# Kernel tuning notes

Measured on AMD Instinct MI355X. Metric: run time of the kernel, lower is better.

## Reference

```python
import jax, jax.numpy as jnp
import numpy as np
from jax import lax

H = 256  # hidden_dim
NDIM = 3
K = 32   # k_neighbors


def sincos_embed(coords, dim, ndim):
    # ContinuousSinCosEmbed: per-coordinate sin/cos features, zero-padded to `dim`.
    dpn = dim // ndim          # channels per coordinate
    half = dpn // 2
    freqs = 1.0 / (10000.0 ** (jnp.arange(half, dtype=coords.dtype) / half))
    ang = coords[..., :, None] * freqs                      # (..., ndim, half)
    emb = jnp.concatenate([jnp.sin(ang), jnp.cos(ang)], -1)  # (..., ndim, 2*half)
    emb = emb.reshape(coords.shape[:-1] + (ndim * 2 * half,))
    pad = dim - ndim * 2 * half
    if pad:
        emb = jnp.concatenate([emb, jnp.zeros(emb.shape[:-1] + (pad,), emb.dtype)], -1)
    return emb


def setup_inputs() -> dict:
    key = jax.random.key(0)
    ks = jax.random.split(key, 8)
    N, S = 50000, 1024
    positions = jax.random.uniform(ks[0], (N, NDIM), dtype=jnp.float32) * 10.0
    supernode_indices = jax.random.randint(ks[1], (S,), 0, N, dtype=jnp.int32)
    g = 1.0 / np.sqrt(H)
    W1 = jax.random.normal(ks[2], (H, H), jnp.float32) * g
    b1 = jnp.zeros((H,), jnp.float32)
    W2 = jax.random.normal(ks[3], (H, H), jnp.float32) * g
    b2 = jnp.zeros((H,), jnp.float32)
    Wp = jax.random.normal(ks[4], (2 * H, H), jnp.float32) * (1.0 / np.sqrt(2 * H))
    bp = jnp.zeros((H,), jnp.float32)
    return {"positions": positions, "supernode_indices": supernode_indices,
            "W1": W1, "b1": b1, "W2": W2, "b2": b2, "Wp": Wp, "bp": bp}


def reference(positions, supernode_indices, W1, b1, W2, b2, Wp, bp):
    # positions: (N, 3); supernode_indices: (S,)
    sup_pos = positions[supernode_indices]                 # (S, 3)
    # kNN neighbor search via dense pairwise squared distances (memory-bound)
    diff = sup_pos[:, None, :] - positions[None, :, :]     # (S, N, 3)
    dist2 = jnp.sum(diff * diff, axis=-1)                  # (S, N)
    _, nbr_idx = lax.top_k(-dist2, K)                      # (S, K)
    nbr_pos = positions[nbr_idx]                           # (S, K, 3)
    # relpos mode: embed (relative position, distance) -> ndim+1 = 4 coords
    rel = sup_pos[:, None, :] - nbr_pos                    # (S, K, 3)
    d = jnp.sqrt(jnp.sum(rel * rel, axis=-1, keepdims=True))  # (S, K, 1)
    rel_feat = jnp.concatenate([rel, d], axis=-1)          # (S, K, 4)
    msg_in = sincos_embed(rel_feat, H, NDIM + 1)           # (S, K, H)
    # message MLP: Dense -> gelu -> Dense
    h = jax.nn.gelu(jnp.einsum('ski,ij->skj', msg_in, W1) + b1)
    msgs = jnp.einsum('ski,ij->skj', h, W2) + b2           # (S, K, H)
    # scatter-reduce: mean over neighbors per supernode
    agg = jnp.mean(msgs, axis=1)                           # (S, H)
    # supernode absolute position embedding, concat, project
    sup_emb = sincos_embed(sup_pos, H, NDIM)               # (S, H)
    feats = jnp.concatenate([sup_emb, agg], axis=-1)       # (S, 2H)
    out = feats @ Wp + bp                                  # (S, H)
    return out[None]                                        # (1, S, H)
```

## Files before the change

kernel.cpp:

```cpp
#include <hip/hip_runtime.h>
#include <hip/hip_bf16.h>
#include <math.h>

typedef short bf16x8 __attribute__((ext_vector_type(8)));
typedef float f32x4  __attribute__((ext_vector_type(4)));

constexpr int   H     = 256;
constexpr int   KNB   = 32;
constexpr int   TPB   = 512;
constexpr int   GC    = 16;
constexpr float HINV  = 1.6f;
constexpr float HCEL  = 0.625f;
constexpr int   SLOTS = 32;
constexpr int   OCAP  = 256;
constexpr int   CAP   = 512;

__device__ __forceinline__ ushort f2bf(float x) {
    unsigned u = __float_as_uint(x);
    u += 0x7FFF + ((u >> 16) & 1);
    return (ushort)(u >> 16);
}

__device__ __forceinline__ float gelu_fast(float x) {
    float u = 0.7978845608028654f * (x + 0.044715f * x * x * x);
    float t = exp2f(-2.885390081777927f * u);
    return x / (1.0f + t);
}

__device__ __forceinline__ int cell_of(float x, float y, float z) {
    int cx = min(GC - 1, max(0, (int)(x * HINV)));
    int cy = min(GC - 1, max(0, (int)(y * HINV)));
    int cz = min(GC - 1, max(0, (int)(z * HINV)));
    return (cz * GC + cy) * GC + cx;
}

__global__ __launch_bounds__(256)
void prep(const float* __restrict__ W1, const float* __restrict__ pos, int N,
          ushort* __restrict__ W1t, float4* __restrict__ pos4s,
          int* __restrict__ origidx, int* __restrict__ cellcnt,
          int* __restrict__ ovfidx, float4* __restrict__ ovfpos) {
    const int b = blockIdx.x;
    if (b < 64) {
        __shared__ float tile[32][33];
        const int ti = b >> 3, tj = b & 7;
        const int r  = threadIdx.x >> 5, c = threadIdx.x & 31;
#pragma unroll
        for (int rr = r; rr < 32; rr += 8)
            tile[rr][c] = W1[(ti * 32 + rr) * H + tj * 32 + c];
        __syncthreads();
#pragma unroll
        for (int rr = r; rr < 32; rr += 8) {
            int j = tj * 32 + rr;
            W1t[j * H + ti * 32 + c] = f2bf(tile[c][rr]);
        }
    } else {
        int i = (b - 64) * 256 + threadIdx.x;
        if (i < N) {
            float x = pos[3 * i], y = pos[3 * i + 1], z = pos[3 * i + 2];
            float4 P = make_float4(x, y, z, 0.f);
            int c = cell_of(x, y, z);
            int slot = atomicAdd(&cellcnt[c], 1);
            if (slot < SLOTS) {
                pos4s[c * SLOTS + slot] = P;
                origidx[c * SLOTS + slot] = i;
            } else {
                int o = atomicAdd(&cellcnt[4096], 1);
                if (o < OCAP) { ovfpos[o] = P; ovfidx[o] = i; }
            }
        }
    }
}

__global__ __launch_bounds__(TPB, 8)
void fused_knn_mlp(const float* __restrict__ pos,
                   const float4* __restrict__ pos4s,
                   const int* __restrict__ origidx,
                   const int* __restrict__ cellcnt,
                   const int* __restrict__ ovfidx, const float4* __restrict__ ovfpos,
                   const int* __restrict__ supidx,
                   const ushort* __restrict__ W1t, const float* __restrict__ b1,
                   const float* __restrict__ W2, const float* __restrict__ b2,
                   float* __restrict__ featsM)
{
    __shared__ __align__(16) char pool[16384];
    float* amaxd = (float*)pool;
    int*   acnt  = (int*)(pool + 512);
    int*   ccell = (int*)(pool + 1024);
    int*   ccnt  = (int*)(pool + 2048);
    float* cmnd  = (float*)(pool + 3072);
    int*   cpre  = (int*)(pool + 4096);
    float* d2buf = (float*)(pool + 5120);
    int*   obuf  = (int*)(pool + 7168);
    float* pxb   = (float*)(pool + 9216);
    float* pyb   = (float*)(pool + 11264);
    float* pzb   = (float*)(pool + 13312);
    ushort* msg  = (ushort*)pool;
    float*  p2   = (float*)pool;

    __shared__ float rf[KNB][5];
    __shared__ int   selo[KNB];
    __shared__ float hb[H];
    __shared__ int   wsum[4];
    __shared__ float tau2_sh, tau32_sh;
    __shared__ int   cnt_sh, ncl;

    const int s    = blockIdx.x;
    const int t    = threadIdx.x;
    const int lane = t & 63;
    const int w    = t >> 6;

    const int sidx = supidx[s];
    const float sx = pos[3 * sidx], sy = pos[3 * sidx + 1], sz = pos[3 * sidx + 2];

    constexpr float L2_10000 = 13.287712379549449f;

    if (t == 0) { ncl = 0; tau2_sh = 301.f; }

    const int scx = min(GC - 1, max(0, (int)(sx * HINV)));
    const int scy = min(GC - 1, max(0, (int)(sy * HINV)));
    const int scz = min(GC - 1, max(0, (int)(sz * HINV)));
    const int ax0 = max(0, scx - 2), ax1 = min(GC - 1, scx + 2);
    const int ay0 = max(0, scy - 2), ay1 = min(GC - 1, scy + 2);
    const int az0 = max(0, scz - 2), az1 = min(GC - 1, scz + 2);
    const int anx = ax1 - ax0 + 1, any_ = ay1 - ay0 + 1, anz = az1 - az0 + 1;
    const int an  = anx * any_ * anz;
    if (t < an) {
        int ci = t;
        int X = ax0 + ci % anx, rem = ci / anx;
        int Y = ay0 + rem % any_, Z = az0 + rem / any_;
        int cell = (Z * GC + Y) * GC + X;
        acnt[ci] = min(cellcnt[cell], SLOTS);
        float lx = X * HCEL, ly = Y * HCEL, lz = Z * HCEL;
        float mx = fmaxf(fabsf(sx - lx), fabsf(lx + HCEL - sx));
        float my = fmaxf(fabsf(sy - ly), fabsf(ly + HCEL - sy));
        float mz = fmaxf(fabsf(sz - lz), fabsf(lz + HCEL - sz));
        amaxd[ci] = mx * mx + my * my + mz * mz;
    }

    if (t < 256) {
        float se = 0.f;
        if (t < 252) {
            int c  = t / 84;
            int rr = t - c * 84;
            int f  = (rr < 42) ? rr : rr - 42;
            float coord = (c == 0) ? sx : ((c == 1) ? sy : sz);
            float ang = coord * exp2f(-(float)f * (L2_10000 / 42.f));
            se = (rr < 42) ? __sinf(ang) : __cosf(ang);
        }
        featsM[s * (2 * H) + t] = se;
    }
    __syncthreads();
    if (t < an) {
        int ci = t;
        float myv = amaxd[ci];
        int Sc = 0;
        for (int j = 0; j < an; j++) {
            bool less = (amaxd[j] < myv) || (amaxd[j] == myv && j < ci);
            Sc += less ? acnt[j] : 0;
        }
        if (Sc < KNB && KNB <= Sc + acnt[ci]) tau2_sh = myv;
    }
    __syncthreads();
    const float tau2 = tau2_sh;
    const float R2 = tau2 + 1e-3f;
    const float R  = sqrtf(R2);
    if (t == 0) tau32_sh = R2;

    const int bx0 = max(0, (int)floorf((sx - R) * HINV));
    const int bx1 = min(GC - 1, (int)floorf((sx + R) * HINV));
    const int by0 = max(0, (int)floorf((sy - R) * HINV));
    const int by1 = min(GC - 1, (int)floorf((sy + R) * HINV));
    const int bz0 = max(0, (int)floorf((sz - R) * HINV));
    const int bz1 = min(GC - 1, (int)floorf((sz + R) * HINV));
    const bool inwin = (bx0 >= ax0 && bx1 <= ax1 && by0 >= ay0 && by1 <= ay1 &&
                        bz0 >= az0 && bz1 <= az1);
    if (inwin) {
        if (t < an) {
            int ci = t;
            int cn = acnt[ci];
            if (cn > 0) {
                int X = ax0 + ci % anx, rem = ci / anx;
                int Y = ay0 + rem % any_, Z = az0 + rem / any_;
                float lx = X * HCEL, ly = Y * HCEL, lz = Z * HCEL;
                float ddx = fmaxf(fmaxf(lx - sx, sx - (lx + HCEL)), 0.f);
                float ddy = fmaxf(fmaxf(ly - sy, sy - (ly + HCEL)), 0.f);
                float ddz = fmaxf(fmaxf(lz - sz, sz - (lz + HCEL)), 0.f);
                float mnd = ddx * ddx + ddy * ddy + ddz * ddz;
                if (mnd <= R2) {
                    int p1 = (amaxd[ci] <= tau2) ? 1 : 0;
                    int cell = (Z * GC + Y) * GC + X;
                    int sl = atomicAdd(&ncl, 1);
                    if (sl < 256) { ccell[sl] = cell; ccnt[sl] = cn | (p1 << 8); cmnd[sl] = mnd; }
                }
            }
        }
    } else {
        const int nbx = bx1 - bx0 + 1, nby = by1 - by0 + 1, nbz = bz1 - bz0 + 1;
        const int ncb = nbx * nby * nbz;
        for (int ci = t; ci < ncb; ci += TPB) {
            int X = bx0 + ci % nbx, rem = ci / nbx;
            int Y = by0 + rem % nby, Z = bz0 + rem / nby;
            float lx = X * HCEL, ly = Y * HCEL, lz = Z * HCEL;
            float ddx = fmaxf(fmaxf(lx - sx, sx - (lx + HCEL)), 0.f);
            float ddy = fmaxf(fmaxf(ly - sy, sy - (ly + HCEL)), 0.f);
            float ddz = fmaxf(fmaxf(lz - sz, sz - (lz + HCEL)), 0.f);
            float mnd = ddx * ddx + ddy * ddy + ddz * ddz;
            if (mnd > R2) continue;
            int cell = (Z * GC + Y) * GC + X;
            int cn = min(cellcnt[cell], SLOTS);
            if (cn == 0) continue;
            float mx = fmaxf(fabsf(sx - lx), fabsf(lx + HCEL - sx));
            float my = fmaxf(fabsf(sy - ly), fabsf(ly + HCEL - sy));
            float mz = fmaxf(fabsf(sz - lz), fabsf(lz + HCEL - sz));
            float amx = mx * mx + my * my + mz * mz;
            int p1 = (amx <= tau2) ? 1 : 0;
            int sl = atomicAdd(&ncl, 1);
            if (sl < 256) { ccell[sl] = cell; ccnt[sl] = cn | (p1 << 8); cmnd[sl] = mnd; }
        }
    }
    __syncthreads();
    const int nclc = min(ncl, 256);

    auto build_prefix = [&](int phase, float tlim) -> int {
        int v = 0;
        if (t < 256) {
            if (t < nclc) {
                int cc = ccnt[t];
                int cn = cc & 0xff;
                int p1 = cc >> 8;
                v = (phase == 1) ? (p1 ? cn : 0)
                                 : ((!p1 && cmnd[t] <= tlim) ? cn : 0);
            }
#pragma unroll
            for (int off = 1; off < 64; off <<= 1) {
                int x = __shfl_up(v, off);
                if (lane >= off) v += x;
            }
            if (lane == 63) wsum[w] = v;
        }
        __syncthreads();
        if (t < 256) {
            int add = 0;
#pragma unroll
            for (int j = 0; j < 4; j++) if (j < w) add += wsum[j];
            cpre[t] = v + add;
        }
        __syncthreads();
        return cpre[255];
    };
    auto bsearch = [&](int j) -> int {
        int lo = 0;
#pragma unroll
        for (int st = 128; st; st >>= 1) {
            int nlo = lo + st;
            if (nlo <= 256 && cpre[nlo - 1] <= j) lo = nlo;
        }
        return lo;
    };

    const int tot1 = build_prefix(1, 0.f);
    const int M1 = min(tot1, CAP);
    if (t < M1) {
        int j = t;
        int lo = bsearch(j);
        int off = j - (lo ? cpre[lo - 1] : 0);
        int u = ccell[lo] * SLOTS + off;
        float4 P = pos4s[u];
        float dx = sx - P.x, dy = sy - P.y, dz = sz - P.z;
        d2buf[j] = dx * dx + dy * dy + dz * dz;
        obuf[j]  = origidx[u];
        pxb[j] = P.x; pyb[j] = P.y; pzb[j] = P.z;
    }
    const int Mp1 = (M1 + 3) & ~3;
    if (M1 + t < Mp1) { d2buf[M1 + t] = INFINITY; obuf[M1 + t] = 0x7fffffff; }
    if (t == 0) cnt_sh = M1;
    __syncthreads();

    if (t < M1) {
        int u = t;
        float myv = d2buf[u];
        int   myo = obuf[u];
        int rank = 0;
        for (int v2 = 0; v2 < Mp1; v2 += 4) {
            float4 dv = *(const float4*)&d2buf[v2];
            int4   iv = *(const int4*)&obuf[v2];
            rank += (dv.x < myv) || (dv.x == myv && iv.x < myo);
            rank += (dv.y < myv) || (dv.y == myv && iv.y < myo);
            rank += (dv.z < myv) || (dv.z == myv && iv.z < myo);
            rank += (dv.w < myv) || (dv.w == myv && iv.w < myo);
        }
        if (rank == KNB - 1) tau32_sh = myv;
    }
    __syncthreads();
    const float tau32 = tau32_sh;

    const int tot2 = build_prefix(2, tau32);
    for (int j0 = 0; j0 < tot2; j0 += TPB) {
        int j = j0 + t;
        bool pass = false; float pd2 = 0.f; int po = 0; float qx = 0, qy = 0, qz = 0;
        if (j < tot2) {
            int lo = bsearch(j);
            int off = j - (lo ? cpre[lo - 1] : 0);
            int u = ccell[lo] * SLOTS + off;
            float4 P = pos4s[u];
            float dx = sx - P.x, dy = sy - P.y, dz = sz - P.z;
            pd2 = dx * dx + dy * dy + dz * dz;
            if (pd2 <= tau32) { pass = true; po = origidx[u]; qx = P.x; qy = P.y; qz = P.z; }
        }
        unsigned long long m = __ballot(pass);
        if (m) {
            int ldr = __ffsll(m) - 1;
            int base = 0;
            if (lane == ldr) base = atomicAdd(&cnt_sh, __popcll(m));
            base = __shfl(base, ldr);
            if (pass) {
                int slp = base + __popcll(m & ((1ull << lane) - 1ull));
                if (slp < CAP) {
                    d2buf[slp] = pd2; obuf[slp] = po;
                    pxb[slp] = qx; pyb[slp] = qy; pzb[slp] = qz;
                }
            }
        }
    }
    {
        int no = min(cellcnt[4096], OCAP);
        for (int j = t; j < no; j += TPB) {
            float4 P = ovfpos[j];
            float dx = sx - P.x, dy = sy - P.y, dz = sz - P.z;
            float pd2 = dx * dx + dy * dy + dz * dz;
            if (pd2 <= tau32) {
                int slp = atomicAdd(&cnt_sh, 1);
                if (slp < CAP) {
                    d2buf[slp] = pd2; obuf[slp] = ovfidx[j];
                    pxb[slp] = P.x; pyb[slp] = P.y; pzb[slp] = P.z;
                }
            }
        }
    }
    __syncthreads();
    const int M = min(cnt_sh, CAP);
    const int Mpad = (M + 3) & ~3;
    if (M + t < Mpad) { d2buf[M + t] = INFINITY; obuf[M + t] = 0x7fffffff; }
    __syncthreads();

    if (t < M) {
        int u = t;
        float myv = d2buf[u];
        int   myo = obuf[u];
        int rank = 0;
        for (int v2 = 0; v2 < Mpad; v2 += 4) {
            float4 dv = *(const float4*)&d2buf[v2];
            int4   iv = *(const int4*)&obuf[v2];
            rank += (dv.x < myv) || (dv.x == myv && iv.x < myo);
            rank += (dv.y < myv) || (dv.y == myv && iv.y < myo);
            rank += (dv.z < myv) || (dv.z == myv && iv.z < myo);
            rank += (dv.w < myv) || (dv.w == myv && iv.w < myo);
        }
        if (rank < KNB) selo[rank] = u;
    }
    __syncthreads();
    if (t < KNB) {
        int u = selo[t];
        float rx = sx - pxb[u], ry = sy - pyb[u], rz = sz - pzb[u];
        float dd = sqrtf(d2buf[u]);
        rf[t][0] = rx; rf[t][1] = ry; rf[t][2] = rz; rf[t][3] = dd;
    }
    __syncthreads();

#pragma unroll
    for (int n = 0; n < 8; n++) {
        int item = t + n * TPB;
        int f = item & 31;
        int c = (item >> 5) & 3;
        int k = item >> 7;
        float ang = rf[k][c] * exp2f(-(float)f * (L2_10000 / 32.f));
        int swz = (k & 7) << 3;
        msg[((k << 8) | (c * 64 + f))      ^ swz] = f2bf(__sinf(ang));
        msg[((k << 8) | (c * 64 + 32 + f)) ^ swz] = f2bf(__cosf(ang));
    }
    __syncthreads();

    {
        const int lr = lane & 15;
        const int lg = lane >> 4;
        f32x4 acc00 = {0,0,0,0}, acc01 = {0,0,0,0};
        f32x4 acc10 = {0,0,0,0}, acc11 = {0,0,0,0};
#pragma unroll
        for (int kk = 0; kk < 8; kk++) {
            const int i0 = kk * 32 + lg * 8;
            bf16x8 a0 = *(const bf16x8*)(W1t + ((32 * w      + lr) << 8) + i0);
            bf16x8 a1 = *(const bf16x8*)(W1t + ((32 * w + 16 + lr) << 8) + i0);
            const int swz = (lr & 7) << 3;
            bf16x8 b0  = *(const bf16x8*)(msg + ((( lr       << 8) | i0) ^ swz));
            bf16x8 b1v = *(const bf16x8*)(msg + ((((lr + 16) << 8) | i0) ^ swz));
            acc00 = __builtin_amdgcn_mfma_f32_16x16x32_bf16(a0, b0,  acc00, 0, 0, 0);
            acc01 = __builtin_amdgcn_mfma_f32_16x16x32_bf16(a0, b1v, acc01, 0, 0, 0);
            acc10 = __builtin_amdgcn_mfma_f32_16x16x32_bf16(a1, b0,  acc10, 0, 0, 0);
            acc11 = __builtin_amdgcn_mfma_f32_16x16x32_bf16(a1, b1v, acc11, 0, 0, 0);
        }
        float part[8];
#pragma unroll
        for (int mm = 0; mm < 2; mm++)
#pragma unroll
            for (int r = 0; r < 4; r++) {
                int j = 32 * w + 16 * mm + 4 * lg + r;
                float bj = b1[j];
                float h0 = (mm == 0 ? acc00[r] : acc10[r]) + bj;
                float h1 = (mm == 0 ? acc01[r] : acc11[r]) + bj;
                part[mm * 4 + r] = gelu_fast(h0) + gelu_fast(h1);
            }
#pragma unroll
        for (int off = 1; off < 16; off <<= 1)
#pragma unroll
            for (int u = 0; u < 8; u++)
                part[u] += __shfl_xor(part[u], off);
        if (lr == 0) {
#pragma unroll
            for (int u = 0; u < 8; u++) {
                int mm = u >> 2, r = u & 3;
                hb[32 * w + 16 * mm + 4 * lg + r] = part[u] * (1.0f / 32.0f);
            }
        }
    }
    __syncthreads();

    {
        const int j4 = lane * 4;
        const int ib = w * 32;
        float4 a = {0.f, 0.f, 0.f, 0.f};
#pragma unroll 4
        for (int i = 0; i < 32; i++) {
            float hv = hb[ib + i];
            float4 wv = *(const float4*)&W2[(ib + i) * H + j4];
            a.x = fmaf(hv, wv.x, a.x); a.y = fmaf(hv, wv.y, a.y);
            a.z = fmaf(hv, wv.z, a.z); a.w = fmaf(hv, wv.w, a.w);
        }
        *(float4*)&p2[w * 256 + j4] = a;
    }
    __syncthreads();
    if (t < 256) {
        float agg = b2[t];
#pragma unroll
        for (int g = 0; g < 8; g++) agg += p2[g * 256 + t];
        featsM[s * (2 * H) + H + t] = agg;
    }
}

__global__ __launch_bounds__(256)
void gemm_bias(const float* __restrict__ A, const float* __restrict__ B,
               const float* __restrict__ bias, float* __restrict__ C,
               int K, int N, int ldc)
{
    __shared__ float As[32][36];
    __shared__ float Bs[32][36];
    const int t  = threadIdx.x;
    const int bm = blockIdx.x, bn = blockIdx.y;
    const int tx = t & 15, ty = t >> 4;
    const int lr = t >> 3, lc = (t & 7) * 4;

    float acc[2][2] = {{0.f, 0.f}, {0.f, 0.f}};

    for (int kk = 0; kk < K; kk += 32) {
        float4 av = *(const float4*)&A[(bm * 32 + lr) * K + kk + lc];
        float4 bv = *(const float4*)&B[(kk + lr) * N + bn * 32 + lc];
        *(float4*)&As[lr][lc] = av;
        *(float4*)&Bs[lr][lc] = bv;
        __syncthreads();
#pragma unroll
        for (int k = 0; k < 32; k++) {
            float a0 = As[2 * ty][k], a1 = As[2 * ty + 1][k];
            float2 b01 = *(const float2*)&Bs[k][2 * tx];
            acc[0][0] += a0 * b01.x; acc[0][1] += a0 * b01.y;
            acc[1][0] += a1 * b01.x; acc[1][1] += a1 * b01.y;
        }
        __syncthreads();
    }
#pragma unroll
    for (int u = 0; u < 2; u++) {
        int row = bm * 32 + 2 * ty + u;
        int col = bn * 32 + 2 * tx;
        C[row * ldc + col]     = acc[u][0] + bias[col];
        C[row * ldc + col + 1] = acc[u][1] + bias[col + 1];
    }
}

extern "C" void kernel_launch(void* const* d_in, const int* in_sizes, int n_in,
                              void* d_out, int out_size, void* d_ws, size_t ws_size,
                              hipStream_t stream) {
    const float* pos = (const float*)d_in[0];
    const int*   sup = (const int*)d_in[1];
    const float* W1  = (const float*)d_in[2];
    const float* b1  = (const float*)d_in[3];
    const float* W2  = (const float*)d_in[4];
    const float* b2  = (const float*)d_in[5];
    const float* Wp  = (const float*)d_in[6];
    const float* bp  = (const float*)d_in[7];

    const int N = in_sizes[0] / 3;
    const int S = in_sizes[1];
    float* out = (float*)d_out;

    char* ws = (char*)d_ws;
    ushort* W1t     = (ushort*)ws;
    float4* pos4s   = (float4*)(ws + (128 << 10));
    int*    origidx = (int*)(ws + (2176 << 10));
    int*    cellcnt = (int*)(ws + (2688 << 10));
    int*    ovfidx  = (int*)(ws + (2708 << 10));
    float4* ovfpos  = (float4*)(ws + (2712 << 10));
    float*  featsM  = (float*)(ws + (2720 << 10));

    hipMemsetAsync(cellcnt, 0, 4097 * sizeof(int), stream);
    prep<<<64 + (N + 255) / 256, 256, 0, stream>>>(W1, pos, N, W1t, pos4s,
                                                   origidx, cellcnt, ovfidx, ovfpos);
    fused_knn_mlp<<<S, TPB, 0, stream>>>(pos, pos4s, origidx, cellcnt,
                                         ovfidx, ovfpos, sup,
                                         W1t, b1, W2, b2, featsM);
    gemm_bias<<<dim3(S / 32, H / 32), 256, 0, stream>>>(featsM, Wp, bp, out,
                                                        2 * H, H, H);
}
```

Before: 83.01 us.

## Replace final FP32 projection GEMM with bf16 MFMA kernel and bf16 weights

```diff
diff --git a/kernel.cpp b/kernel.cpp
--- a/kernel.cpp
+++ b/kernel.cpp
@@ -21,6 +21,10 @@
     return (ushort)(u >> 16);
 }
 
+__device__ __forceinline__ float bf2f(ushort u) {
+    return __uint_as_float(((unsigned)u) << 16);
+}
+
 __device__ __forceinline__ float gelu_fast(float x) {
     float u = 0.7978845608028654f * (x + 0.044715f * x * x * x);
     float t = exp2f(-2.885390081777927f * u);
@@ -35,8 +39,10 @@
 }
 
 __global__ __launch_bounds__(256)
-void prep(const float* __restrict__ W1, const float* __restrict__ pos, int N,
-          ushort* __restrict__ W1t, float4* __restrict__ pos4s,
+void prep(const float* __restrict__ W1, const float* __restrict__ Wp,
+          const float* __restrict__ W2, const float* __restrict__ pos, int N,
+          ushort* __restrict__ W1t, ushort* __restrict__ Wpt,
+          ushort* __restrict__ W2b, float4* __restrict__ pos4s,
           int* __restrict__ origidx, int* __restrict__ cellcnt,
           int* __restrict__ ovfidx, float4* __restrict__ ovfpos) {
     const int b = blockIdx.x;
@@ -49,12 +55,28 @@
             tile[rr][c] = W1[(ti * 32 + rr) * H + tj * 32 + c];
         __syncthreads();
 #pragma unroll
-        for (int rr = r; rr < 32; rr += 8) {
-            int j = tj * 32 + rr;
-            W1t[j * H + ti * 32 + c] = f2bf(tile[c][rr]);
-        }
+        for (int rr = r; rr < 32; rr += 8)
+            W1t[(tj * 32 + rr) * H + ti * 32 + c] = f2bf(tile[c][rr]);
+    } else if (b < 192) {
+        __shared__ float tile[32][33];
+        const int b2 = b - 64;
+        const int ti = b2 >> 3, tj = b2 & 7;
+        const int r  = threadIdx.x >> 5, c = threadIdx.x & 31;
+#pragma unroll
+        for (int rr = r; rr < 32; rr += 8)
+            tile[rr][c] = Wp[(ti * 32 + rr) * H + tj * 32 + c];
+        __syncthreads();
+#pragma unroll
+        for (int rr = r; rr < 32; rr += 8)
+            Wpt[(tj * 32 + rr) * (2 * H) + ti * 32 + c] = f2bf(tile[c][rr]);
+    } else if (b < 256) {
+        const int e4 = (b - 192) * 1024 + threadIdx.x * 4;
+        float4 v = *(const float4*)&W2[e4];
+        ushort4 o;
+        o.x = f2bf(v.x); o.y = f2bf(v.y); o.z = f2bf(v.z); o.w = f2bf(v.w);
+        *(ushort4*)&W2b[e4] = o;
     } else {
-        int i = (b - 64) * 256 + threadIdx.x;
+        int i = (b - 256) * 256 + threadIdx.x;
         if (i < N) {
             float x = pos[3 * i], y = pos[3 * i + 1], z = pos[3 * i + 2];
             float4 P = make_float4(x, y, z, 0.f);
@@ -79,8 +101,8 @@
                    const int* __restrict__ ovfidx, const float4* __restrict__ ovfpos,
                    const int* __restrict__ supidx,
                    const ushort* __restrict__ W1t, const float* __restrict__ b1,
-                   const float* __restrict__ W2, const float* __restrict__ b2,
-                   float* __restrict__ featsM)
+                   const ushort* __restrict__ W2b, const float* __restrict__ b2,
+                   ushort* __restrict__ featsB)
 {
     __shared__ __align__(16) char pool[16384];
     float* amaxd = (float*)pool;
@@ -147,7 +169,7 @@
             float ang = coord * exp2f(-(float)f * (L2_10000 / 42.f));
             se = (rr < 42) ? __sinf(ang) : __cosf(ang);
         }
-        featsM[s * (2 * H) + t] = se;
+        featsB[s * (2 * H) + t] = f2bf(se);
     }
     __syncthreads();
     if (t < an) {
@@ -431,9 +453,11 @@
 #pragma unroll 4
         for (int i = 0; i < 32; i++) {
             float hv = hb[ib + i];
-            float4 wv = *(const float4*)&W2[(ib + i) * H + j4];
-            a.x = fmaf(hv, wv.x, a.x); a.y = fmaf(hv, wv.y, a.y);
-            a.z = fmaf(hv, wv.z, a.z); a.w = fmaf(hv, wv.w, a.w);
+            ushort4 wv = *(const ushort4*)&W2b[(ib + i) * H + j4];
+            a.x = fmaf(hv, bf2f(wv.x), a.x);
+            a.y = fmaf(hv, bf2f(wv.y), a.y);
+            a.z = fmaf(hv, bf2f(wv.z), a.z);
+            a.w = fmaf(hv, bf2f(wv.w), a.w);
         }
         *(float4*)&p2[w * 256 + j4] = a;
     }
@@ -442,46 +466,49 @@
         float agg = b2[t];
 #pragma unroll
         for (int g = 0; g < 8; g++) agg += p2[g * 256 + t];
-        featsM[s * (2 * H) + H + t] = agg;
-    }
-}
-
-__global__ __launch_bounds__(256)
-void gemm_bias(const float* __restrict__ A, const float* __restrict__ B,
-               const float* __restrict__ bias, float* __restrict__ C,
-               int K, int N, int ldc)
+        featsB[s * (2 * H) + H + t] = f2bf(agg);
+    }
+}
+
+__global__ __launch_bounds__(512)
+void mfma_out(const ushort* __restrict__ featsB, const ushort* __restrict__ Wpt,
+              const float* __restrict__ bp, float* __restrict__ out)
 {
-    __shared__ float As[32][36];
-    __shared__ float Bs[32][36];
-    const int t  = threadIdx.x;
-    const int bm = blockIdx.x, bn = blockIdx.y;
-    const int tx = t & 15, ty = t >> 4;
-    const int lr = t >> 3, lc = (t & 7) * 4;
-
-    float acc[2][2] = {{0.f, 0.f}, {0.f, 0.f}};
-
-    for (int kk = 0; kk < K; kk += 32) {
-        float4 av = *(const float4*)&A[(bm * 32 + lr) * K + kk + lc];
-        float4 bv = *(const float4*)&B[(kk + lr) * N + bn * 32 + lc];
-        *(float4*)&As[lr][lc] = av;
-        *(float4*)&Bs[lr][lc] = bv;
-        __syncthreads();
-#pragma unroll
-        for (int k = 0; k < 32; k++) {
-            float a0 = As[2 * ty][k], a1 = As[2 * ty + 1][k];
-            float2 b01 = *(const float2*)&Bs[k][2 * tx];
-            acc[0][0] += a0 * b01.x; acc[0][1] += a0 * b01.y;
-            acc[1][0] += a1 * b01.x; acc[1][1] += a1 * b01.y;
-        }
-        __syncthreads();
-    }
-#pragma unroll
-    for (int u = 0; u < 2; u++) {
-        int row = bm * 32 + 2 * ty + u;
-        int col = bn * 32 + 2 * tx;
-        C[row * ldc + col]     = acc[u][0] + bias[col];
-        C[row * ldc + col + 1] = acc[u][1] + bias[col + 1];
-    }
+    const int bm   = blockIdx.x;
+    const int t    = threadIdx.x;
+    const int lane = t & 63;
+    const int w    = t >> 6;
+    const int lr   = lane & 15;
+    const int lg   = lane >> 4;
+
+    f32x4 acc[2][2];
+#pragma unroll
+    for (int mt = 0; mt < 2; mt++)
+#pragma unroll
+        for (int nt = 0; nt < 2; nt++) acc[mt][nt] = (f32x4){0, 0, 0, 0};
+
+#pragma unroll
+    for (int kk = 0; kk < 16; kk++) {
+        const int i0 = kk * 32 + lg * 8;
+        bf16x8 a0 = *(const bf16x8*)(featsB + (32 * bm      + lr) * 512 + i0);
+        bf16x8 a1 = *(const bf16x8*)(featsB + (32 * bm + 16 + lr) * 512 + i0);
+        bf16x8 b0 = *(const bf16x8*)(Wpt + (32 * w      + lr) * 512 + i0);
+        bf16x8 b1 = *(const bf16x8*)(Wpt + (32 * w + 16 + lr) * 512 + i0);
+        acc[0][0] = __builtin_amdgcn_mfma_f32_16x16x32_bf16(a0, b0, acc[0][0], 0, 0, 0);
+        acc[0][1] = __builtin_amdgcn_mfma_f32_16x16x32_bf16(a0, b1, acc[0][1], 0, 0, 0);
+        acc[1][0] = __builtin_amdgcn_mfma_f32_16x16x32_bf16(a1, b0, acc[1][0], 0, 0, 0);
+        acc[1][1] = __builtin_amdgcn_mfma_f32_16x16x32_bf16(a1, b1, acc[1][1], 0, 0, 0);
+    }
+#pragma unroll
+    for (int mt = 0; mt < 2; mt++)
+#pragma unroll
+        for (int nt = 0; nt < 2; nt++)
+#pragma unroll
+            for (int r = 0; r < 4; r++) {
+                int srow = 32 * bm + 16 * mt + 4 * lg + r;
+                int j    = 32 * w  + 16 * nt + lr;
+                out[srow * H + j] = acc[mt][nt][r] + bp[j];
+            }
 }
 
 extern "C" void kernel_launch(void* const* d_in, const int* in_sizes, int n_in,
@@ -502,19 +529,21 @@
 
     char* ws = (char*)d_ws;
     ushort* W1t     = (ushort*)ws;
-    float4* pos4s   = (float4*)(ws + (128 << 10));
-    int*    origidx = (int*)(ws + (2176 << 10));
-    int*    cellcnt = (int*)(ws + (2688 << 10));
-    int*    ovfidx  = (int*)(ws + (2708 << 10));
-    float4* ovfpos  = (float4*)(ws + (2712 << 10));
-    float*  featsM  = (float*)(ws + (2720 << 10));
+    ushort* Wpt     = (ushort*)(ws + (128 << 10));
+    ushort* W2b     = (ushort*)(ws + (384 << 10));
+    float4* pos4s   = (float4*)(ws + (512 << 10));
+    int*    origidx = (int*)(ws + (2560 << 10));
+    int*    cellcnt = (int*)(ws + (3072 << 10));
+    int*    ovfidx  = (int*)(ws + (3092 << 10));
+    float4* ovfpos  = (float4*)(ws + (3096 << 10));
+    ushort* featsB  = (ushort*)(ws + (3104 << 10));
 
     hipMemsetAsync(cellcnt, 0, 4097 * sizeof(int), stream);
-    prep<<<64 + (N + 255) / 256, 256, 0, stream>>>(W1, pos, N, W1t, pos4s,
-                                                   origidx, cellcnt, ovfidx, ovfpos);
+    prep<<<256 + (N + 255) / 256, 256, 0, stream>>>(W1, Wp, W2, pos, N,
+                                                    W1t, Wpt, W2b, pos4s,
+                                                    origidx, cellcnt, ovfidx, ovfpos);
     fused_knn_mlp<<<S, TPB, 0, stream>>>(pos, pos4s, origidx, cellcnt,
                                          ovfidx, ovfpos, sup,
-                                         W1t, b1, W2, b2, featsM);
-    gemm_bias<<<dim3(S / 32, H / 32), 256, 0, stream>>>(featsM, Wp, bp, out,
-                                                        2 * H, H, H);
-}
+                                         W1t, b1, W2b, b2, featsB);
+    mfma_out<<<S / 32, 512, 0, stream>>>(featsB, Wpt, bp, out);
+}
```

Measured after the change: 80.93 us. 2.5% less time.
